# Optimization experiments

Hardware: AMD Instinct MI355X
Metric: run time of the kernel (lower is better)

The kernel has to match this reference:

```python
import jax, jax.numpy as jnp
import numpy as np

B, C1, C2, H, W = 4, 96, 96, 40, 40
DE, DI, R, N, K, E, TOPK = 192, 192, 6, 16, 4, 4, 2
EPS_BN = 1e-5
EPS_LN = 1e-5


def conv1x1(x, w):
    # x: (B,C,H,W), w: (O,C)
    return jnp.einsum('bchw,oc->bohw', x, w)


def dwconv3(x, w, b):
    # depthwise 3x3, w: (C,1,3,3)
    C = x.shape[1]
    y = jax.lax.conv_general_dilated(x, w, (1, 1), 'SAME',
                                     dimension_numbers=('NCHW', 'OIHW', 'NCHW'),
                                     feature_group_count=C)
    return y + b[None, :, None, None]


def bn_eval(x, g, b):
    # BatchNorm2d in eval mode with running_mean=0, running_var=1
    s = g / jnp.sqrt(1.0 + EPS_BN)
    return x * s[None, :, None, None] + b[None, :, None, None]


def layernorm(x, g, b):
    m = x.mean(-1, keepdims=True)
    xc = x - m
    v = (xc * xc).mean(-1, keepdims=True)
    return xc / jnp.sqrt(v + EPS_LN) * g + b


def gelu(x):
    return jax.nn.gelu(x, approximate=False)


def selective_scan(xs, dts, As, Bs, Cs):
    # xs, dts: (B,K,D,L); As: (K,D,N); Bs, Cs: (B,K,N,L)
    Bb, Kk, Dd, L = xs.shape
    Nn = As.shape[-1]
    xs_l = jnp.moveaxis(xs, -1, 0)   # (L,B,K,D)
    dts_l = jnp.moveaxis(dts, -1, 0)
    Bs_l = jnp.moveaxis(Bs, -1, 0)   # (L,B,K,N)
    Cs_l = jnp.moveaxis(Cs, -1, 0)
    h0 = jnp.zeros((Bb, Kk, Dd, Nn), xs.dtype)

    def step(h, inp):
        x_t, dt_t, B_t, C_t = inp
        dA = jnp.exp(dt_t[..., None] * As)                  # (B,K,D,N)
        h = h * dA + (dt_t * x_t)[..., None] * B_t[:, :, None, :]
        y = jnp.einsum('bkdn,bkn->bkd', h, C_t)
        return h, y

    _, ys = jax.lax.scan(step, h0, (xs_l, dts_l, Bs_l, Cs_l))
    return jnp.moveaxis(ys, 0, -1)   # (B,K,D,L)


def ss2d(x, in_proj_w, conv_w, conv_b, x_proj_w, dt_w, dt_b, A_logs, Ds,
         onorm_g, onorm_b, out_proj_w):
    # x: (B, C2, H, W)
    xz = conv1x1(x, in_proj_w)                      # (B, 2*DE, H, W)
    xx, z = jnp.split(xz, 2, axis=1)
    z1 = gelu(z)
    xx = gelu(dwconv3(xx, conv_w, conv_b))          # (B, DE, H, W)

    Bb, Dd, Hh, Ww = xx.shape
    L = Hh * Ww
    x_hw = xx.reshape(Bb, Dd, L)
    x_wh = xx.transpose(0, 1, 3, 2).reshape(Bb, Dd, L)
    xs = jnp.stack([x_hw, x_wh, x_hw[..., ::-1], x_wh[..., ::-1]], axis=1)  # (B,K,D,L)

    x_dbl = jnp.einsum('bkdl,kcd->bkcl', xs, x_proj_w)
    dts_r = x_dbl[:, :, :R]
    Bs = x_dbl[:, :, R:R + N]
    Cs = x_dbl[:, :, R + N:]
    dts = jnp.einsum('bkrl,kdr->bkdl', dts_r, dt_w)
    dts = jax.nn.softplus(dts + dt_b[None, :, :, None])
    As = -jnp.exp(A_logs.reshape(K, Dd, N))

    ys = selective_scan(xs, dts, As, Bs, Cs)
    ys = ys + Ds.reshape(K, Dd)[None, :, :, None] * xs

    # CrossMerge
    y = ys[:, 0] + ys[:, 2, :, ::-1]
    y_wh = ys[:, 1] + ys[:, 3, :, ::-1]
    y = y + y_wh.reshape(Bb, Dd, Ww, Hh).transpose(0, 1, 3, 2).reshape(Bb, Dd, L)

    y = layernorm(y.transpose(0, 2, 1), onorm_g, onorm_b)   # (B,L,D)
    y = y.reshape(Bb, Hh, Ww, Dd).transpose(0, 3, 1, 2)     # (B,D,H,W)
    y = y * z1
    return conv1x1(y, out_proj_w)


def moe(x, router_w, router_b, dw_w, dw_b, pw_w, pw_b):
    Bb = x.shape[0]
    g = x.mean(axis=(2, 3))                                 # (B,C)
    logits = g @ router_w.T + router_b
    prob = jax.nn.softmax(logits / 2.0, axis=-1)
    tp, ti = jax.lax.top_k(prob, TOPK)
    tp = tp / tp.sum(-1, keepdims=True)
    wmat = jnp.zeros((Bb, E), x.dtype).at[jnp.arange(Bb)[:, None], ti].add(tp)
    out = jnp.zeros_like(x)
    for e in range(E):
        h = gelu(dwconv3(x, dw_w[e], dw_b[e]))
        h = conv1x1(h, pw_w[e]) + pw_b[e][None, :, None, None]
        out = out + wmat[:, e][:, None, None, None] * h
    return out


def _forward(x, proj_w, bn0_g, bn0_b, ls_fc1_w, ls_fc1_b, ls_bn_g, ls_bn_b,
             ls_fc2_w, ls_fc2_b, ls_fc3_w, ls_fc3_b, n1_g, n1_b,
             in_proj_w, conv_w, conv_b, x_proj_w, dt_w, dt_b, A_logs, Ds,
             onorm_g, onorm_b, out_proj_w, n2_g, n2_b,
             router_w, router_b, moe_dw_w, moe_dw_b, moe_pw_w, moe_pw_b):
    x = jax.nn.silu(bn_eval(conv1x1(x, proj_w), bn0_g, bn0_b))
    res1 = x
    # LSBlock
    h = dwconv3(x, ls_fc1_w, ls_fc1_b)
    h = bn_eval(h, ls_bn_g, ls_bn_b)
    h = conv1x1(h, ls_fc2_w) + ls_fc2_b[None, :, None, None]
    h = gelu(h)
    h = conv1x1(h, ls_fc3_w) + ls_fc3_b[None, :, None, None]
    x1 = x + h
    x1 = ss2d(bn_eval(x1, n1_g, n1_b), in_proj_w, conv_w, conv_b, x_proj_w,
              dt_w, dt_b, A_logs, Ds, onorm_g, onorm_b, out_proj_w)
    x = res1 + x1
    x2 = moe(bn_eval(x, n2_g, n2_b), router_w, router_b,
             moe_dw_w, moe_dw_b, moe_pw_w, moe_pw_b)
    return x + x2


def setup_inputs() -> dict:
    key = jax.random.key(0)
    ks = jax.random.split(key, 16)
    rn = lambda k, shape, s: jax.random.normal(k, shape, jnp.float32) * s
    ones = lambda *s: jnp.ones(s, jnp.float32)
    zeros = lambda *s: jnp.zeros(s, jnp.float32)
    return {
        'x': jax.random.normal(ks[0], (B, C1, H, W), jnp.float32),
        'proj_w': rn(ks[1], (C2, C1), 0.1),
        'bn0_g': ones(C2), 'bn0_b': zeros(C2),
        'ls_fc1_w': rn(ks[2], (C2, 1, 3, 3), 0.2), 'ls_fc1_b': zeros(C2),
        'ls_bn_g': ones(C2), 'ls_bn_b': zeros(C2),
        'ls_fc2_w': rn(ks[3], (C2, C2), 0.1), 'ls_fc2_b': zeros(C2),
        'ls_fc3_w': rn(ks[4], (C2, C2), 0.1), 'ls_fc3_b': zeros(C2),
        'n1_g': ones(C2), 'n1_b': zeros(C2),
        'in_proj_w': rn(ks[5], (2 * DE, C2), 0.1),
        'conv_w': rn(ks[6], (DE, 1, 3, 3), 0.2), 'conv_b': zeros(DE),
        'x_proj_w': rn(ks[7], (K, R + 2 * N, DI), 0.1),
        'dt_w': rn(ks[8], (K, DI, R), 0.3),
        'dt_b': rn(ks[9], (K, DI), 0.5),
        'A_logs': rn(ks[10], (K * DI, N), 0.5),
        'Ds': ones(K * DI),
        'onorm_g': ones(DI), 'onorm_b': zeros(DI),
        'out_proj_w': rn(ks[11], (C2, DE), 0.1),
        'n2_g': ones(C2), 'n2_b': zeros(C2),
        'router_w': rn(ks[12], (E, C2), 0.1), 'router_b': zeros(E),
        'moe_dw_w': rn(ks[13], (E, C2, 1, 3, 3), 0.2), 'moe_dw_b': zeros(E, C2),
        'moe_pw_w': rn(ks[14], (E, C2, C2), 0.1), 'moe_pw_b': zeros(E, C2),
    }


def reference(x, proj_w, bn0_g, bn0_b, ls_fc1_w, ls_fc1_b, ls_bn_g, ls_bn_b,
              ls_fc2_w, ls_fc2_b, ls_fc3_w, ls_fc3_b, n1_g, n1_b,
              in_proj_w, conv_w, conv_b, x_proj_w, dt_w, dt_b, A_logs, Ds,
              onorm_g, onorm_b, out_proj_w, n2_g, n2_b,
              router_w, router_b, moe_dw_w, moe_dw_b, moe_pw_w, moe_pw_b):
    return _forward(x, proj_w, bn0_g, bn0_b, ls_fc1_w, ls_fc1_b, ls_bn_g, ls_bn_b,
                    ls_fc2_w, ls_fc2_b, ls_fc3_w, ls_fc3_b, n1_g, n1_b,
                    in_proj_w, conv_w, conv_b, x_proj_w, dt_w, dt_b, A_logs, Ds,
                    onorm_g, onorm_b, out_proj_w, n2_g, n2_b,
                    router_w, router_b, moe_dw_w, moe_dw_b, moe_pw_w, moe_pw_b)
```

## Files before the change

kernel.cpp:

```cpp
#include <hip/hip_runtime.h>
#include <hip/hip_bf16.h>
#include <math.h>

#define BB 4
#define CC 96
#define LL 1600
#define DD 192
#define KK 4
#define RR 6
#define NN 16
#define EE 4
#define NCH 40
#define CLEN 40

typedef __hip_bfloat16 bf16;

__device__ __forceinline__ float geluf(float x){ return 0.5f*x*(1.0f+erff(x*0.70710678118654752440f)); }
__device__ __forceinline__ float softplusf(float x){ return (x>20.0f)? x : __logf(1.0f+__expf(x)); }
#define BNS rsqrtf(1.0f + 1e-5f)
#define LOG2E 1.44269504088896340736f

__device__ __forceinline__ int xpos(int k, int l){
  if (k==0) return l;
  if (k==2) return LL-1-l;
  int t = (k==1)? l : (LL-1-l);
  return (t%40)*40 + t/40;
}

struct P33 { const void* p[33]; };
#define NTOT 790660
__device__ const int g_cum[34] = {
  0, 614400, 623616, 623712, 623808, 624672, 624768, 624864, 624960,
  634176, 634272, 643488, 643584, 643680, 643776, 680640, 682368, 682560,
  711744, 716352, 717120, 729408, 730176, 730368, 730560, 748992, 749088,
  749184, 749568, 749572, 753028, 753412, 790276, 790660
};

__global__ void k_convert(P33 ps, float* cv){
  bool f32 = (((const unsigned*)ps.p[21])[0] == 0x3F800000u);
  int idx = blockIdx.x*256 + threadIdx.x;
  if (idx >= NTOT) return;
  int lo=0, hi=33;
  while (lo+1<hi){ int mid=(lo+hi)>>1; if (idx >= g_cum[mid]) lo=mid; else hi=mid; }
  int local = idx - g_cum[lo];
  float v = f32 ? ((const float*)ps.p[lo])[local]
                : __bfloat162float(((const bf16*)ps.p[lo])[local]);
  cv[idx] = v;
}

__global__ void k_proj(const float* x, const float* w, const float* g, const float* b_, float* out){
  __shared__ float lx[96*64];
  int bid = blockIdx.x;
  int ot = bid%3, lt = (bid/3)%25, b = bid/75;
  int l0 = lt*64, ob = ot*32;
  const float* inb = x + b*CC*LL;
  for (int i=threadIdx.x; i<96*64; i+=256) lx[i] = inb[(i>>6)*LL + l0 + (i&63)];
  __syncthreads();
  int oq = threadIdx.x>>5, lq = threadIdx.x&31;
  float acc[4][2] = {};
  #pragma unroll 4
  for (int c=0;c<96;c++){
    float x0 = lx[c*64+lq], x1 = lx[c*64+lq+32];
    #pragma unroll
    for (int jo=0;jo<4;jo++){
      float wv = w[(ob+oq+8*jo)*CC + c];
      acc[jo][0] += wv*x0; acc[jo][1] += wv*x1;
    }
  }
  #pragma unroll
  for (int jo=0;jo<4;jo++){
    int o = ob+oq+8*jo;
    float sc = g[o]*BNS, bb = b_[o];
    #pragma unroll
    for (int jl=0;jl<2;jl++){
      float v = acc[jo][jl]*sc + bb;
      out[(b*CC+o)*LL + l0+lq+32*jl] = v/(1.0f+__expf(-v));
    }
  }
}

__global__ void k_fc_gelu(const float* in, const float* w, const float* bias, float* out){
  __shared__ float lx[96*64];
  int bid = blockIdx.x;
  int ot = bid%3, lt = (bid/3)%25, b = bid/75;
  int l0 = lt*64, ob = ot*32;
  const float* inb = in + b*CC*LL;
  for (int i=threadIdx.x; i<96*64; i+=256) lx[i] = inb[(i>>6)*LL + l0 + (i&63)];
  __syncthreads();
  int oq = threadIdx.x>>5, lq = threadIdx.x&31;
  float acc[4][2] = {};
  #pragma unroll 4
  for (int c=0;c<96;c++){
    float x0 = lx[c*64+lq], x1 = lx[c*64+lq+32];
    #pragma unroll
    for (int jo=0;jo<4;jo++){
      float wv = w[(ob+oq+8*jo)*CC + c];
      acc[jo][0] += wv*x0; acc[jo][1] += wv*x1;
    }
  }
  #pragma unroll
  for (int jo=0;jo<4;jo++){
    int o = ob+oq+8*jo;
    float bb = bias[o];
    out[(b*CC+o)*LL + l0+lq]    = geluf(acc[jo][0]+bb);
    out[(b*CC+o)*LL + l0+lq+32] = geluf(acc[jo][1]+bb);
  }
}

__global__ void k_fc_res_bn(const float* in, const float* w, const float* bias, const float* res,
                            const float* g, const float* b_, float* out){
  __shared__ float lx[96*64];
  int bid = blockIdx.x;
  int ot = bid%3, lt = (bid/3)%25, b = bid/75;
  int l0 = lt*64, ob = ot*32;
  const float* inb = in + b*CC*LL;
  for (int i=threadIdx.x; i<96*64; i+=256) lx[i] = inb[(i>>6)*LL + l0 + (i&63)];
  __syncthreads();
  int oq = threadIdx.x>>5, lq = threadIdx.x&31;
  float acc[4][2] = {};
  #pragma unroll 4
  for (int c=0;c<96;c++){
    float x0 = lx[c*64+lq], x1 = lx[c*64+lq+32];
    #pragma unroll
    for (int jo=0;jo<4;jo++){
      float wv = w[(ob+oq+8*jo)*CC + c];
      acc[jo][0] += wv*x0; acc[jo][1] += wv*x1;
    }
  }
  #pragma unroll
  for (int jo=0;jo<4;jo++){
    int o = ob+oq+8*jo;
    float bb = bias[o], sc = g[o]*BNS, b2 = b_[o];
    #pragma unroll
    for (int jl=0;jl<2;jl++){
      int pos = (b*CC+o)*LL + l0+lq+32*jl;
      float v = acc[jo][jl] + bb + res[pos];
      out[pos] = v*sc + b2;
    }
  }
}

__global__ void k_inproj(const float* in, const float* w, float* xxp, float* z1){
  __shared__ float lx[96*64];
  int bid = blockIdx.x;
  int ot = bid%12, lt = (bid/12)%25, b = bid/300;
  int l0 = lt*64, ob = ot*32;
  const float* inb = in + b*CC*LL;
  for (int i=threadIdx.x; i<96*64; i+=256) lx[i] = inb[(i>>6)*LL + l0 + (i&63)];
  __syncthreads();
  int oq = threadIdx.x>>5, lq = threadIdx.x&31;
  float acc[4][2] = {};
  #pragma unroll 4
  for (int c=0;c<96;c++){
    float x0 = lx[c*64+lq], x1 = lx[c*64+lq+32];
    #pragma unroll
    for (int jo=0;jo<4;jo++){
      float wv = w[(ob+oq+8*jo)*CC + c];
      acc[jo][0] += wv*x0; acc[jo][1] += wv*x1;
    }
  }
  if (ot < 6){
    #pragma unroll
    for (int jo=0;jo<4;jo++){
      int oc = ob+oq+8*jo;
      xxp[(b*DD+oc)*LL + l0+lq]    = acc[jo][0];
      xxp[(b*DD+oc)*LL + l0+lq+32] = acc[jo][1];
    }
  } else {
    __syncthreads();
    #pragma unroll
    for (int jo=0;jo<4;jo++){
      int oo = oq+8*jo;
      lx[lq*33 + oo]      = geluf(acc[jo][0]);
      lx[(lq+32)*33 + oo] = geluf(acc[jo][1]);
    }
    __syncthreads();
    int zb = ob - 192;
    for (int i=threadIdx.x; i<64*32; i+=256){
      int u = i>>5, oo = i&31;
      z1[(b*LL + l0+u)*DD + zb + oo] = lx[u*33 + oo];
    }
  }
}

__global__ void k_ssconv(const float* in, const float* w, const float* bias, float* out){
  int idx = blockIdx.x*256 + threadIdx.x;
  if (idx >= BB*DD*LL) return;
  int l = idx%LL, d = (idx/LL)%DD, b = idx/(LL*DD);
  int y = l/40, x0 = l%40;
  const float* ip = in + (b*DD+d)*LL;
  float acc = 0.f;
  #pragma unroll
  for (int ky=0;ky<3;ky++){
    int yy = y+ky-1; if (yy<0||yy>=40) continue;
    #pragma unroll
    for (int kx=0;kx<3;kx++){
      int xx = x0+kx-1; if (xx<0||xx>=40) continue;
      acc += w[d*9+ky*3+kx] * ip[yy*40+xx];
    }
  }
  out[idx] = geluf(acc + bias[d]);
}

__global__ void k_dwbn(const float* in, const float* w, const float* bias, const float* g, const float* b_, float* out){
  int idx = blockIdx.x*256 + threadIdx.x;
  if (idx >= BB*CC*LL) return;
  int l = idx%LL, c = (idx/LL)%CC, b = idx/(LL*CC);
  int y = l/40, x0 = l%40;
  const float* ip = in + (b*CC+c)*LL;
  float acc = 0.f;
  #pragma unroll
  for (int ky=0;ky<3;ky++){
    int yy = y+ky-1; if (yy<0||yy>=40) continue;
    #pragma unroll
    for (int kx=0;kx<3;kx++){
      int xx = x0+kx-1; if (xx<0||xx>=40) continue;
      acc += w[c*9+ky*3+kx] * ip[yy*40+xx];
    }
  }
  acc += bias[c];
  out[idx] = acc*(g[c]*BNS) + b_[c];
}

__global__ void k_xsxw(const float* xx, float* xs, float* xw1, float* Y){
  __shared__ float sm[40*41];
  int bid = blockIdx.x;
  if (bid < 1200){
    float (*t)[33] = (float(*)[33])sm;
    int lt = bid % 50, dt = (bid/50)%6, b = bid/300;
    int l0 = lt*32, d0 = dt*32;
    int tx = threadIdx.x & 31, ty = threadIdx.x >> 5;
    #pragma unroll
    for (int j=0;j<4;j++){
      int dd = ty + 8*j;
      t[dd][tx] = xx[(b*DD + d0+dd)*LL + l0 + tx];
    }
    __syncthreads();
    #pragma unroll
    for (int j=0;j<4;j++){
      int ll = ty + 8*j;
      int l = l0 + ll;
      float v = t[tx][ll];
      int lw = (l%40)*40 + l/40;
      xs[((b*2+0)*LL + l )*DD + d0 + tx] = v;
      xs[((b*2+1)*LL + lw)*DD + d0 + tx] = v;
    }
  } else {
    int bd = bid - 1200;
    const float* ip = xx + bd*LL;
    float* op = xw1 + bd*LL;
    for (int i=threadIdx.x; i<LL; i+=256) sm[(i/40)*41 + (i%40)] = ip[i];
    float* yz0 = Y + bd*LL;
    for (int i=threadIdx.x; i<LL; i+=256) yz0[i] = 0.f;
    __syncthreads();
    for (int i=threadIdx.x; i<LL; i+=256) op[i] = sm[(i%40)*41 + (i/40)];
  }
}

__global__ void k_xdbl(const float* xx, const float* xw1, const float* w, float* xd){
  __shared__ float lt_[32*41];
  int bid = blockIdx.x;
  int tt = bid % 50, bk = bid / 50;
  int k = bk & 3, b = bk >> 2;
  int t0 = tt*32;
  int cg = threadIdx.x >> 5, tl = threadIdx.x & 31;
  int t = t0 + tl;
  int row = (k<2)? t : (LL-1-t);
  const float* base = ((k&1)? xw1 : xx) + b*DD*LL + row;
  const float* wp[5];
  #pragma unroll
  for (int j=0;j<5;j++){
    int c = cg + 8*j; if (c>37) c = 37;
    wp[j] = w + (k*38+c)*DD;
  }
  float acc[5] = {};
  for (int d=0; d<DD; d++){
    float xv = base[d*LL];
    #pragma unroll
    for (int j=0;j<5;j++) acc[j] += wp[j][d]*xv;
  }
  #pragma unroll
  for (int j=0;j<5;j++){
    int c = cg + 8*j;
    if (c < 38) lt_[tl*41 + c] = acc[j];
  }
  __syncthreads();
  float* ob = xd + (bk*LL + t0)*40;
  for (int i=threadIdx.x; i<32*40; i+=256){
    int tr = i/40, col = i%40;
    float v;
    if (col < 32)      v = lt_[tr*41 + col + 6];
    else if (col < 38) v = lt_[tr*41 + col - 32];
    else               v = 0.f;
    ob[i] = v;
  }
}

__global__ void k_scan1(const float* xs, const float* xd, const float* dtw, const float* dtb,
                        const float* Alog, float* Pb, float* Sb){
  __shared__ float slab[CLEN*44];
  __shared__ float ldt[64*41];
  __shared__ float ldtw[64*7];
  __shared__ float ldtb[64];
  int bid = blockIdx.x;
  int dt3 = bid % 3;
  int c   = (bid/3) % NCH;
  int bk  = bid/(3*NCH);
  int k = bk & 3, b = bk >> 2;
  int d0 = dt3*64;
  const float* xrow0 = xd + (bk*LL + c*CLEN)*40;
  for (int i=threadIdx.x; i<CLEN*40; i+=256)
    slab[(i/40)*44 + (i%40)] = xrow0[i];
  for (int i=threadIdx.x; i<64*RR; i+=256)
    ldtw[(i/RR)*7 + (i%RR)] = dtw[(k*DD+d0 + i/RR)*RR + (i%RR)];
  if (threadIdx.x < 64) ldtb[threadIdx.x] = dtb[k*DD+d0+threadIdx.x];
  __syncthreads();
  for (int i=threadIdx.x; i<64*CLEN; i+=256){
    int j = i>>6, dd = i&63;
    float dtr = ldtb[dd];
    #pragma unroll
    for (int q=0;q<RR;q++) dtr += ldtw[dd*7+q]*slab[j*44+32+q];
    ldt[dd*41+j] = softplusf(dtr);
  }
  __syncthreads();
  int lane = threadIdx.x & 63;
  int d16 = lane & 15, g = lane >> 4;
  int dd = (threadIdx.x>>6)*16 + d16;
  int d = d0 + dd;
  int kd = k*DD + d;
  float A2[4], P[4]={1.f,1.f,1.f,1.f}, S[4]={0.f,0.f,0.f,0.f};
  #pragma unroll
  for (int n=0;n<4;n++) A2[n] = -expf(Alog[kd*NN + g*4 + n])*LOG2E;
  const float* xsb = xs + ((b*2)+(k&1))*LL*DD;
  bool rev = (k>=2);
  int t0 = c*CLEN;
  for (int j=0;j<CLEN;j++){
    int t = t0+j;
    int row = rev? (LL-1-t) : t;
    float dt = ldt[dd*41 + j];
    float4 B4 = *(const float4*)(&slab[j*44 + g*4]);
    float xv = xsb[row*DD + d];
    float u = dt*xv;
    float Ba[4] = {B4.x,B4.y,B4.z,B4.w};
    #pragma unroll
    for (int n=0;n<4;n++){
      float dA = exp2f(dt*A2[n]);
      P[n] *= dA;
      S[n] = S[n]*dA + u*Ba[n];
    }
  }
  int off = ((bk*DD + d)*NCH + c)*NN + g*4;
  *(float4*)(Pb+off) = make_float4(P[0],P[1],P[2],P[3]);
  *(float4*)(Sb+off) = make_float4(S[0],S[1],S[2],S[3]);
}

__global__ void k_scanmid(float* Pb, const float* Sb){
  int idx = blockIdx.x*256 + threadIdx.x;
  if (idx >= BB*KK*DD*NN) return;
  int n = idx%NN, bkd = idx/NN;
  float h = 0.f;
  for (int c=0;c<NCH;c++){
    int o = (bkd*NCH + c)*NN + n;
    float p = Pb[o], s = Sb[o];
    Pb[o] = h;
    h = p*h + s;
  }
}

__global__ void k_scan2(const float* xs, const float* xd, const float* dtw, const float* dtb,
                        const float* Alog, const float* Hin, const float* Ds, float* Y){
  __shared__ float slab[CLEN*44];
  __shared__ float ldt[64*41];
  __shared__ float ldtw[64*7];
  __shared__ float ldtb[64];
  int bid = blockIdx.x;
  int dt3 = bid % 3;
  int c   = (bid/3) % NCH;
  int bk  = bid/(3*NCH);
  int k = bk & 3, b = bk >> 2;
  int d0 = dt3*64;
  const float* xrow0 = xd + (bk*LL + c*CLEN)*40;
  for (int i=threadIdx.x; i<CLEN*40; i+=256)
    slab[(i/40)*44 + (i%40)] = xrow0[i];
  for (int i=threadIdx.x; i<64*RR; i+=256)
    ldtw[(i/RR)*7 + (i%RR)] = dtw[(k*DD+d0 + i/RR)*RR + (i%RR)];
  if (threadIdx.x < 64) ldtb[threadIdx.x] = dtb[k*DD+d0+threadIdx.x];
  __syncthreads();
  for (int i=threadIdx.x; i<64*CLEN; i+=256){
    int j = i>>6, dd = i&63;
    float dtr = ldtb[dd];
    #pragma unroll
    for (int q=0;q<RR;q++) dtr += ldtw[dd*7+q]*slab[j*44+32+q];
    ldt[dd*41+j] = softplusf(dtr);
  }
  __syncthreads();
  int lane = threadIdx.x & 63;
  int d16 = lane & 15, g = lane >> 4;
  int dd = (threadIdx.x>>6)*16 + d16;
  int d = d0 + dd;
  int kd = k*DD + d;
  int off = ((bk*DD + d)*NCH + c)*NN + g*4;
  float4 h4 = *(const float4*)(Hin+off);
  float h[4] = {h4.x, h4.y, h4.z, h4.w};
  float A2[4];
  #pragma unroll
  for (int n=0;n<4;n++) A2[n] = -expf(Alog[kd*NN + g*4 + n])*LOG2E;
  float Dv = Ds[kd];
  const float* xsb = xs + ((b*2)+(k&1))*LL*DD;
  float* yb = Y + b*LL*DD;
  bool rev = (k>=2);
  int t0 = c*CLEN;
  for (int j=0;j<CLEN;j++){
    int t = t0+j;
    int row = rev? (LL-1-t) : t;
    float dt = ldt[dd*41 + j];
    float4 B4 = *(const float4*)(&slab[j*44 + g*4]);
    float4 C4 = *(const float4*)(&slab[j*44 + 16 + g*4]);
    float xv = xsb[row*DD + d];
    float u = dt*xv;
    float Ba[4] = {B4.x,B4.y,B4.z,B4.w};
    float Ca[4] = {C4.x,C4.y,C4.z,C4.w};
    float y = 0.f;
    #pragma unroll
    for (int n=0;n<4;n++){
      float dA = exp2f(dt*A2[n]);
      h[n] = h[n]*dA + u*Ba[n];
      y += h[n]*Ca[n];
    }
    y += __shfl_xor(y, 16, 64);
    y += __shfl_xor(y, 32, 64);
    if (g==0){
      int p = xpos(k, t);
      atomicAdd(&yb[p*DD + d], y + Dv*xv);
    }
  }
}

__global__ void k_ln(const float* Y, const float* og, const float* ob, const float* z1, float* yz, float* gv){
  if (blockIdx.x == 0){
    for (int i=threadIdx.x; i<BB*CC; i+=256) gv[i] = 0.f;
  }
  int r = blockIdx.x*4 + (threadIdx.x >> 6);
  int lane = threadIdx.x & 63;
  const float* yp = Y + r*DD;
  float v0 = yp[lane], v1 = yp[lane+64], v2 = yp[lane+128];
  float s = v0+v1+v2;
  #pragma unroll
  for (int off=32; off>0; off>>=1) s += __shfl_xor(s, off, 64);
  float m = s*(1.0f/DD);
  float t0=v0-m, t1=v1-m, t2=v2-m;
  float vv = t0*t0+t1*t1+t2*t2;
  #pragma unroll
  for (int off=32; off>0; off>>=1) vv += __shfl_xor(vv, off, 64);
  float rs = rsqrtf(vv*(1.0f/DD) + 1e-5f);
  #pragma unroll
  for (int i=0;i<3;i++){
    int d = lane + 64*i;
    float t = (i==0?t0:(i==1?t1:t2));
    yz[r*DD + d] = (t*rs*og[d] + ob[d]) * z1[r*DD + d];
  }
}

__global__ void k_outproj(const float* yz, const float* w, const float* res, const float* g, const float* b_,
                          float* x2, float* xb, float* gv){
  __shared__ float lx[64*193];
  int bid = blockIdx.x;
  int ot = bid%3, lt = (bid/3)%25, b = bid/75;
  int l0 = lt*64, ob = ot*32;
  const float* src = yz + (b*LL + l0)*DD;
  for (int i=threadIdx.x; i<64*192; i+=256) lx[(i/192)*193 + (i%192)] = src[i];
  __syncthreads();
  int oq = threadIdx.x>>5, lq = threadIdx.x&31;
  float acc[4][2] = {};
  #pragma unroll 4
  for (int c=0;c<192;c++){
    float x0 = lx[lq*193 + c], x1 = lx[(lq+32)*193 + c];
    #pragma unroll
    for (int jo=0;jo<4;jo++){
      float wv = w[(ob+oq+8*jo)*DD + c];
      acc[jo][0] += wv*x0; acc[jo][1] += wv*x1;
    }
  }
  #pragma unroll
  for (int jo=0;jo<4;jo++){
    int o = ob+oq+8*jo;
    float sc = g[o]*BNS, b2 = b_[o];
    float xb0 = 0.f, xb1 = 0.f;
    {
      int pos = (b*CC+o)*LL + l0+lq;
      float v = res[pos] + acc[jo][0];
      x2[pos] = v; xb0 = v*sc + b2; xb[pos] = xb0;
      pos += 32;
      float v2 = res[pos] + acc[jo][1];
      x2[pos] = v2; xb1 = v2*sc + b2; xb[pos] = xb1;
    }
    float sv = xb0 + xb1;
    #pragma unroll
    for (int off=1; off<32; off<<=1) sv += __shfl_xor(sv, off, 64);
    if (lq == 0) atomicAdd(&gv[b*CC + o], sv*(1.0f/LL));
  }
}

__global__ void k_moedw(const float* xb, const float* dw, const float* db, float* he){
  int idx = blockIdx.x*256 + threadIdx.x;
  if (idx >= BB*CC*LL) return;
  int l = idx%LL, c = (idx/LL)%CC, b = idx/(LL*CC);
  int y = l/40, x0 = l%40;
  const float* ip = xb + (b*CC+c)*LL;
  float v[9];
  #pragma unroll
  for (int ky=0;ky<3;ky++){
    #pragma unroll
    for (int kx=0;kx<3;kx++){
      int yy=y+ky-1, xx=x0+kx-1;
      v[ky*3+kx] = (yy<0||yy>=40||xx<0||xx>=40)? 0.f : ip[yy*40+xx];
    }
  }
  #pragma unroll
  for (int e=0;e<EE;e++){
    const float* wp = dw + (e*CC+c)*9;
    float acc = db[e*CC+c];
    #pragma unroll
    for (int q=0;q<9;q++) acc += wp[q]*v[q];
    he[((e*BB+b)*CC+c)*LL+l] = geluf(acc);
  }
}

__global__ void k_final(const float* he, const float* pw, const float* pb,
                        const float* gv, const float* rw, const float* rb,
                        const float* x2, void* out, const void* dsraw){
  __shared__ float lx[96*64];
  bool f32 = (((const unsigned*)dsraw)[0] == 0x3F800000u);
  int bid = blockIdx.x;
  int ot = bid%3, lt = (bid/3)%25, b = bid/75;
  int l0 = lt*64, ob = ot*32;
  float wmv[EE];
  {
    float lg[EE];
    for (int e=0;e<EE;e++){
      float a = rb[e];
      for (int cc2=0;cc2<CC;cc2++) a += gv[b*CC+cc2]*rw[e*CC+cc2];
      lg[e] = a*0.5f;
    }
    float mx = lg[0];
    for (int e=1;e<EE;e++) mx = fmaxf(mx, lg[e]);
    float p[EE], s = 0.f;
    for (int e=0;e<EE;e++){ p[e] = __expf(lg[e]-mx); s += p[e]; }
    for (int e=0;e<EE;e++) p[e] /= s;
    int i1 = 0;
    for (int e=1;e<EE;e++) if (p[e] > p[i1]) i1 = e;
    int i2 = -1;
    for (int e=0;e<EE;e++){ if (e==i1) continue; if (i2<0 || p[e]>p[i2]) i2 = e; }
    float tot = p[i1]+p[i2];
    for (int e=0;e<EE;e++) wmv[e] = 0.f;
    wmv[i1] = p[i1]/tot;
    wmv[i2] = p[i2]/tot;
  }
  int oq = threadIdx.x>>5, lq = threadIdx.x&31;
  float acc[4][2] = {};
  float bias[4] = {0.f,0.f,0.f,0.f};
  for (int e=0;e<EE;e++){
    float wv = wmv[e];
    if (wv == 0.f) continue;
    __syncthreads();
    const float* hb = he + (e*BB+b)*CC*LL;
    for (int i=threadIdx.x; i<96*64; i+=256) lx[i] = hb[(i>>6)*LL + l0 + (i&63)];
    __syncthreads();
    float ae[4][2] = {};
    #pragma unroll 4
    for (int c=0;c<96;c++){
      float x0 = lx[c*64+lq], x1 = lx[c*64+lq+32];
      #pragma unroll
      for (int jo=0;jo<4;jo++){
        float wvw = pw[(e*CC+ob+oq+8*jo)*CC + c];
        ae[jo][0] += wvw*x0; ae[jo][1] += wvw*x1;
      }
    }
    #pragma unroll
    for (int jo=0;jo<4;jo++){
      acc[jo][0] += wv*ae[jo][0];
      acc[jo][1] += wv*ae[jo][1];
      bias[jo] += wv*pb[e*CC+ob+oq+8*jo];
    }
  }
  #pragma unroll
  for (int jo=0;jo<4;jo++){
    int o = ob+oq+8*jo;
    #pragma unroll
    for (int jl=0;jl<2;jl++){
      int pos = (b*CC+o)*LL + l0+lq+32*jl;
      float v = x2[pos] + acc[jo][jl] + bias[jo];
      if (f32) ((float*)out)[pos] = v;
      else     ((bf16*)out)[pos] = __float2bfloat16(v);
    }
  }
}

extern "C" void kernel_launch(void* const* d_in, const int* in_sizes, int n_in,
                              void* d_out, int out_size, void* d_ws, size_t ws_size,
                              hipStream_t stream) {
  static const int cum[34] = {
    0, 614400, 623616, 623712, 623808, 624672, 624768, 624864, 624960,
    634176, 634272, 643488, 643584, 643680, 643776, 680640, 682368, 682560,
    711744, 716352, 717120, 729408, 730176, 730368, 730560, 748992, 749088,
    749184, 749568, 749572, 753028, 753412, 790276, 790660
  };
  float* ws = (float*)d_ws;
  const float* cv[33];
  P33 ps;
  for (int i=0;i<33;i++){ ps.p[i] = d_in[i]; cv[i] = ws + cum[i]; }

  const float* c_x    = cv[0];
  const float* c_pw   = cv[1];
  const float* c_bn0g = cv[2];
  const float* c_bn0b = cv[3];
  const float* c_f1w  = cv[4];
  const float* c_f1b  = cv[5];
  const float* c_lbg  = cv[6];
  const float* c_lbb  = cv[7];
  const float* c_f2w  = cv[8];
  const float* c_f2b  = cv[9];
  const float* c_f3w  = cv[10];
  const float* c_f3b  = cv[11];
  const float* c_n1g  = cv[12];
  const float* c_n1b  = cv[13];
  const float* c_ipw  = cv[14];
  const float* c_cw   = cv[15];
  const float* c_cb   = cv[16];
  const float* c_xpw  = cv[17];
  const float* c_dtw  = cv[18];
  const float* c_dtb  = cv[19];
  const float* c_al   = cv[20];
  const float* c_ds   = cv[21];
  const float* c_ong  = cv[22];
  const float* c_onb  = cv[23];
  const float* c_opw  = cv[24];
  const float* c_n2g  = cv[25];
  const float* c_n2b  = cv[26];
  const float* c_rw   = cv[27];
  const float* c_rb   = cv[28];
  const float* c_mdw  = cv[29];
  const float* c_mdb  = cv[30];
  const float* c_mpw  = cv[31];
  const float* c_mpb  = cv[32];

  float* R   = ws +   790784;
  float* T1  = ws +  1405184;
  float* X1  = T1;
  float* X2  = T1;
  float* T2  = ws +  2019584;
  float* XB  = T2;
  float* XW1 = T1;
  float* XXP = ws +  2633984;
  float* Y   = XXP;
  float* Z1  = ws +  3862784;
  float* XX  = ws +  5091584;
  float* YZ  = XX;
  float* XS  = ws +  6320384;
  float* HE  = XS;
  float* XD  = ws +  8777984;
  float* GV  = XD;
  float* PB  = ws +  9801984;
  float* SB  = ws + 11768064;

  const int T = 256;
  k_convert  <<<(NTOT+T-1)/T, T, 0, stream>>>(ps, ws);
  k_proj     <<<300, T, 0, stream>>>(c_x, c_pw, c_bn0g, c_bn0b, R);
  k_dwbn     <<<(BB*CC*LL+T-1)/T, T, 0, stream>>>(R, c_f1w, c_f1b, c_lbg, c_lbb, T1);
  k_fc_gelu  <<<300, T, 0, stream>>>(T1, c_f2w, c_f2b, T2);
  k_fc_res_bn<<<300, T, 0, stream>>>(T2, c_f3w, c_f3b, R, c_n1g, c_n1b, X1);
  k_inproj   <<<1200, T, 0, stream>>>(X1, c_ipw, XXP, Z1);
  k_ssconv   <<<(BB*DD*LL+T-1)/T, T, 0, stream>>>(XXP, c_cw, c_cb, XX);
  k_xsxw     <<<1968, T, 0, stream>>>(XX, XS, XW1, Y);
  k_xdbl     <<<BB*KK*50, T, 0, stream>>>(XX, XW1, c_xpw, XD);
  k_scan1    <<<BB*KK*NCH*3, T, 0, stream>>>(XS, XD, c_dtw, c_dtb, c_al, PB, SB);
  k_scanmid  <<<(BB*KK*DD*NN+T-1)/T, T, 0, stream>>>(PB, SB);
  k_scan2    <<<BB*KK*NCH*3, T, 0, stream>>>(XS, XD, c_dtw, c_dtb, c_al, PB, c_ds, Y);
  k_ln       <<<1600, T, 0, stream>>>(Y, c_ong, c_onb, Z1, YZ, GV);
  k_outproj  <<<300, T, 0, stream>>>(YZ, c_opw, R, c_n2g, c_n2b, X2, XB, GV);
  k_moedw    <<<(BB*CC*LL+T-1)/T, T, 0, stream>>>(XB, c_mdw, c_mdb, HE);
  k_final    <<<300, T, 0, stream>>>(HE, c_mpw, c_mpb, GV, c_rw, c_rb, X2, d_out, d_in[21]);
}
```

Baseline: 393.5 us.

## Share x_proj input slab between forward and reversed scan directions

The x_proj kernel now handles directions k and k+2 together, since the reversed direction reads the same spatial rows as its forward pair. Each block stages a 32x192 input slab in shared memory once and computes both projections, with float4 weight loads. The reversed direction's output is written with flipped row order. This halves global input reads and the block count, at the cost of a larger shared-memory footprint and fewer blocks in flight.

```diff
diff --git a/kernel.cpp b/kernel.cpp
--- a/kernel.cpp
+++ b/kernel.cpp
@@ -258,41 +258,72 @@
 }
 
 __global__ void k_xdbl(const float* xx, const float* xw1, const float* w, float* xd){
-  __shared__ float lt_[32*41];
-  int bid = blockIdx.x;
-  int tt = bid % 50, bk = bid / 50;
-  int k = bk & 3, b = bk >> 2;
+  __shared__ float slab[32*193];
+  int bid = blockIdx.x;
+  int tt = bid % 50;
+  int s  = (bid/50) & 1;
+  int b  = bid/100;
   int t0 = tt*32;
-  int cg = threadIdx.x >> 5, tl = threadIdx.x & 31;
-  int t = t0 + tl;
-  int row = (k<2)? t : (LL-1-t);
-  const float* base = ((k&1)? xw1 : xx) + b*DD*LL + row;
-  const float* wp[5];
-  #pragma unroll
-  for (int j=0;j<5;j++){
-    int c = cg + 8*j; if (c>37) c = 37;
-    wp[j] = w + (k*38+c)*DD;
-  }
-  float acc[5] = {};
-  for (int d=0; d<DD; d++){
-    float xv = base[d*LL];
-    #pragma unroll
-    for (int j=0;j<5;j++) acc[j] += wp[j][d]*xv;
-  }
+  const float* src = (s? xw1 : xx) + b*DD*LL;
+  for (int i=threadIdx.x; i<192*32; i+=256){
+    int d = i>>5, tl2 = i&31;
+    slab[tl2*193 + d] = src[d*LL + t0 + tl2];
+  }
+  __syncthreads();
+  int cg = threadIdx.x>>5, tl = threadIdx.x&31;
+  const float* w0 = w + (s*38)*DD;
+  const float* w2 = w + ((s+2)*38)*DD;
+  float accA[5] = {}, accB[5] = {};
+  int cidx[5];
+  #pragma unroll
+  for (int j=0;j<5;j++){ int c = cg + 8*j; cidx[j] = (c>37)? 37 : c; }
+  const float* sp = slab + tl*193;
+  for (int d=0; d<DD; d+=4){
+    float s0 = sp[d], s1 = sp[d+1], s2 = sp[d+2], s3 = sp[d+3];
+    #pragma unroll
+    for (int j=0;j<5;j++){
+      float4 wa = *(const float4*)(w0 + cidx[j]*DD + d);
+      float4 wb = *(const float4*)(w2 + cidx[j]*DD + d);
+      accA[j] += wa.x*s0 + wa.y*s1 + wa.z*s2 + wa.w*s3;
+      accB[j] += wb.x*s0 + wb.y*s1 + wb.z*s2 + wb.w*s3;
+    }
+  }
+  __syncthreads();
+  float* lt0 = slab;
+  float* lt1 = slab + 32*41;
   #pragma unroll
   for (int j=0;j<5;j++){
     int c = cg + 8*j;
-    if (c < 38) lt_[tl*41 + c] = acc[j];
-  }
-  __syncthreads();
-  float* ob = xd + (bk*LL + t0)*40;
-  for (int i=threadIdx.x; i<32*40; i+=256){
-    int tr = i/40, col = i%40;
-    float v;
-    if (col < 32)      v = lt_[tr*41 + col + 6];
-    else if (col < 38) v = lt_[tr*41 + col - 32];
-    else               v = 0.f;
-    ob[i] = v;
+    if (c < 38){
+      lt0[tl*41 + c] = accA[j];
+      lt1[tl*41 + c] = accB[j];
+    }
+  }
+  __syncthreads();
+  {
+    int bk = b*KK + s;
+    float* ob = xd + (bk*LL + t0)*40;
+    for (int i=threadIdx.x; i<32*40; i+=256){
+      int tr = i/40, col = i%40;
+      float v;
+      if (col < 32)      v = lt0[tr*41 + col + 6];
+      else if (col < 38) v = lt0[tr*41 + col - 32];
+      else               v = 0.f;
+      ob[i] = v;
+    }
+  }
+  {
+    int bk = b*KK + s + 2;
+    float* ob = xd + (bk*LL + (LL-32-t0))*40;
+    for (int i=threadIdx.x; i<32*40; i+=256){
+      int tr = i/40, col = i%40;
+      int tloc = 31 - tr;
+      float v;
+      if (col < 32)      v = lt1[tloc*41 + col + 6];
+      else if (col < 38) v = lt1[tloc*41 + col - 32];
+      else               v = 0.f;
+      ob[i] = v;
+    }
   }
 }
 
@@ -672,7 +703,7 @@
   k_inproj   <<<1200, T, 0, stream>>>(X1, c_ipw, XXP, Z1);
   k_ssconv   <<<(BB*DD*LL+T-1)/T, T, 0, stream>>>(XXP, c_cw, c_cb, XX);
   k_xsxw     <<<1968, T, 0, stream>>>(XX, XS, XW1, Y);
-  k_xdbl     <<<BB*KK*50, T, 0, stream>>>(XX, XW1, c_xpw, XD);
+  k_xdbl     <<<BB*2*50, T, 0, stream>>>(XX, XW1, c_xpw, XD);
   k_scan1    <<<BB*KK*NCH*3, T, 0, stream>>>(XS, XD, c_dtw, c_dtb, c_al, PB, SB);
   k_scanmid  <<<(BB*KK*DD*NN+T-1)/T, T, 0, stream>>>(PB, SB);
   k_scan2    <<<BB*KK*NCH*3, T, 0, stream>>>(XS, XD, c_dtw, c_dtb, c_al, PB, c_ds, Y);
```

New measurement: 380.4 us. -3.3%, faster.
